# Optimization experiments

Hardware: AMD Instinct MI355X
Metric: run time of the kernel (lower is better)

Reference implementation:

```python
import jax, jax.numpy as jnp
import numpy as np

USER = 100000
ITEM = 200000
N = USER + ITEM
LATDIM = 64
N_LAYERS = 3
N_EDGES = 9600000


def setup_inputs() -> dict:
    key = jax.random.key(0)
    k1, k2, k3, k4, k5 = jax.random.split(key, 5)
    # xavier_uniform for [N, latdim]: bound = sqrt(6/(fan_in+fan_out))
    bu = float(np.sqrt(6.0 / (USER + LATDIM)))
    bi = float(np.sqrt(6.0 / (ITEM + LATDIM)))
    uEmbeds = jax.random.uniform(k1, (USER, LATDIM), jnp.float32, -bu, bu)
    iEmbeds = jax.random.uniform(k2, (ITEM, LATDIM), jnp.float32, -bi, bi)
    edge_row = jax.random.randint(k3, (N_EDGES,), 0, N, dtype=jnp.int32)
    edge_col = jax.random.randint(k4, (N_EDGES,), 0, N, dtype=jnp.int32)
    edge_val = jax.random.uniform(k5, (N_EDGES,), jnp.float32) * 0.01
    return {"uEmbeds": uEmbeds, "iEmbeds": iEmbeds,
            "edge_row": edge_row, "edge_col": edge_col, "edge_val": edge_val}


def _spmm(row, col, val, x):
    # sparse adj (COO) @ dense x: gather cols, scale, scatter-add to rows
    msgs = x[col] * val[:, None]                 # [E, D]
    return jax.ops.segment_sum(msgs, row, num_segments=N)  # [N, D]


def reference(uEmbeds, iEmbeds, edge_row, edge_col, edge_val):
    # forward_gcn: multi-layer propagation, sum of all layer embeddings
    embeds = jnp.concatenate([uEmbeds, iEmbeds], axis=0)  # [N, D]
    acc = embeds
    cur = embeds
    for _ in range(N_LAYERS):
        cur = _spmm(edge_row, edge_col, edge_val, cur)
        acc = acc + cur
    return acc[:USER], acc[USER:]
```

## Files before the change

kernel.cpp:

```cpp
#include <hip/hip_runtime.h>
#include <hip/hip_bf16.h>

#define USER_N   100000
#define ITEM_N   200000
#define N_NODES  300000
#define LATDIM   64
#define N_EDGES  9600000
#define N_LAYERS 3

#define B_SHIFT  6
#define B_ROWS   64
#define NB       ((N_NODES + B_ROWS - 1) / B_ROWS)
#define GPART    512
#define EPB      ((N_EDGES + GPART - 1) / GPART)
#define SEG      5
#define CAP      3072

__device__ __forceinline__ unsigned short f2bf(float f) {
    unsigned int u = __float_as_uint(f);
    u += 0x7FFFu + ((u >> 16) & 1u);
    return (unsigned short)(u >> 16);
}
__device__ __forceinline__ float bf2f(unsigned short h) {
    return __uint_as_float(((unsigned int)h) << 16);
}

__global__ void cvt_concat_kernel(const float* __restrict__ u,
                                  const float* __restrict__ it,
                                  ushort4* __restrict__ cur0,
                                  int n4u, int n4total) {
    int stride = gridDim.x * blockDim.x;
    for (int i = blockIdx.x * blockDim.x + threadIdx.x; i < n4total; i += stride) {
        float4 v = (i < n4u) ? ((const float4*)u)[i]
                             : ((const float4*)it)[i - n4u];
        ushort4 o;
        o.x = f2bf(v.x); o.y = f2bf(v.y); o.z = f2bf(v.z); o.w = f2bf(v.w);
        cur0[i] = o;
    }
}

__device__ __forceinline__ int slice_of(int blk) {
    return ((blk & 7) << 6) | (blk >> 3);
}

__global__ void p1_count_kernel(const int* __restrict__ row,
                                int* __restrict__ cnt) {
    __shared__ int h[NB];
    int s = slice_of(blockIdx.x), t = threadIdx.x;
    for (int i = t; i < NB; i += 256) h[i] = 0;
    __syncthreads();
    int e0 = s * EPB;
    int e1 = e0 + EPB; if (e1 > N_EDGES) e1 = N_EDGES;
    for (int e = e0 + t; e < e1; e += 256)
        atomicAdd(&h[row[e] >> B_SHIFT], 1);
    __syncthreads();
    for (int i = t; i < NB; i += 256)
        cnt[i * GPART + s] = h[i];
}

__global__ void p2_scan_kernel(int* __restrict__ cnt, int* __restrict__ btot) {
    __shared__ int lds[GPART];
    int b = blockIdx.x, t = threadIdx.x;
    int v = cnt[b * GPART + t];
    lds[t] = v;
    __syncthreads();
    for (int off = 1; off < GPART; off <<= 1) {
        int add = (t >= off) ? lds[t - off] : 0;
        __syncthreads();
        lds[t] += add;
        __syncthreads();
    }
    cnt[b * GPART + t] = lds[t] - v;
    if (t == GPART - 1) btot[b] = lds[t];
}

__global__ void p3_scan_kernel(const int* __restrict__ btot,
                               int* __restrict__ bstart,
                               int* __restrict__ rowPtr) {
    __shared__ int lds[1024];
    int t = threadIdx.x;
    int base = t * SEG;
    int loc[SEG];
    int s = 0;
    #pragma unroll
    for (int k = 0; k < SEG; ++k) {
        int i = base + k;
        int v = (i < NB) ? btot[i] : 0;
        loc[k] = v;
        s += v;
    }
    lds[t] = s;
    __syncthreads();
    for (int off = 1; off < 1024; off <<= 1) {
        int add = (t >= off) ? lds[t - off] : 0;
        __syncthreads();
        lds[t] += add;
        __syncthreads();
    }
    int ex = lds[t] - s;
    #pragma unroll
    for (int k = 0; k < SEG; ++k) {
        int i = base + k;
        if (i < NB) bstart[i] = ex;
        ex += loc[k];
    }
    if (t == 1023) {
        bstart[NB] = lds[1023];
        rowPtr[N_NODES] = N_EDGES;
    }
}

__global__ void p4_scatter_kernel(const int*   __restrict__ row,
                                  const int*   __restrict__ col,
                                  const float* __restrict__ val,
                                  const int*   __restrict__ bstart,
                                  const int*   __restrict__ cnt,
                                  int2*        __restrict__ temp) {
    __shared__ int cur[NB];
    int s = slice_of(blockIdx.x), t = threadIdx.x;
    for (int i = t; i < NB; i += 256)
        cur[i] = bstart[i] + cnt[i * GPART + s];
    __syncthreads();
    int e0 = s * EPB;
    int e1 = e0 + EPB; if (e1 > N_EDGES) e1 = N_EDGES;
    for (int e = e0 + t; e < e1; e += 256) {
        int r = row[e];
        int b = r >> B_SHIFT;
        int pos = atomicAdd(&cur[b], 1);
        temp[pos] = make_int2(((r & (B_ROWS - 1)) << 19) | col[e],
                              __float_as_int(val[e]));
    }
}

__global__ __launch_bounds__(256)
void bucket_sort_kernel(const int*  __restrict__ bstart,
                        const int2* __restrict__ temp,
                        int2*       __restrict__ colval,
                        int*        __restrict__ rowPtr) {
    __shared__ int hist[B_ROWS];
    __shared__ int curs[B_ROWS];
    __shared__ int2 stage[CAP];
    int b = blockIdx.x, t = threadIdx.x;
    int beg = bstart[b];
    int end = bstart[b + 1];
    int n = end - beg;

    if (t < B_ROWS) hist[t] = 0;
    __syncthreads();
    for (int i = beg + t; i < end; i += 256)
        atomicAdd(&hist[((unsigned)temp[i].x) >> 19], 1);
    __syncthreads();

    if (t < B_ROWS) {
        int v = hist[t];
        int inc = v;
        #pragma unroll
        for (int d = 1; d < B_ROWS; d <<= 1) {
            int o = __shfl_up(inc, d, 64);
            if (t >= d) inc += o;
        }
        int ex = inc - v;
        curs[t] = ex;
        int r = (b << B_SHIFT) + t;
        if (r < N_NODES) rowPtr[r] = beg + ex;
    }
    __syncthreads();

    for (int i = beg + t; i < end; i += 256) {
        int2 kv = temp[i];
        int rl = ((unsigned)kv.x) >> 19;
        int p  = atomicAdd(&curs[rl], 1);
        int2 out = make_int2(kv.x & 0x7FFFF, kv.y);
        if (p < CAP) stage[p] = out;
        else         colval[beg + p] = out;
    }
    __syncthreads();

    int lim = (n < CAP) ? n : CAP;
    for (int i = t; i < lim; i += 256)
        colval[beg + i] = stage[i];
}

__global__ void spmm_bf16_kernel(const int*  __restrict__ rp,
                                 const int2* __restrict__ cv,
                                 const ushort4* __restrict__ x4,
                                 ushort4*       __restrict__ y4) {
    int g = (blockIdx.x * blockDim.x + threadIdx.x) >> 4;
    if (g >= N_NODES) return;
    int q = threadIdx.x & 15;
    int beg = rp[g];
    int end = rp[g + 1];

    float s0 = 0.f, s1 = 0.f, s2 = 0.f, s3 = 0.f;
    int i = beg;
    for (; i + 4 <= end; i += 4) {
        int2 c0 = cv[i], c1 = cv[i + 1], c2 = cv[i + 2], c3 = cv[i + 3];
        ushort4 g0 = x4[(size_t)c0.x * 16 + q];
        ushort4 g1 = x4[(size_t)c1.x * 16 + q];
        ushort4 g2 = x4[(size_t)c2.x * 16 + q];
        ushort4 g3 = x4[(size_t)c3.x * 16 + q];
        float v0 = __int_as_float(c0.y), v1 = __int_as_float(c1.y);
        float v2 = __int_as_float(c2.y), v3 = __int_as_float(c3.y);
        s0 += bf2f(g0.x) * v0; s1 += bf2f(g0.y) * v0;
        s2 += bf2f(g0.z) * v0; s3 += bf2f(g0.w) * v0;
        s0 += bf2f(g1.x) * v1; s1 += bf2f(g1.y) * v1;
        s2 += bf2f(g1.z) * v1; s3 += bf2f(g1.w) * v1;
        s0 += bf2f(g2.x) * v2; s1 += bf2f(g2.y) * v2;
        s2 += bf2f(g2.z) * v2; s3 += bf2f(g2.w) * v2;
        s0 += bf2f(g3.x) * v3; s1 += bf2f(g3.y) * v3;
        s2 += bf2f(g3.z) * v3; s3 += bf2f(g3.w) * v3;
    }
    for (; i < end; ++i) {
        int2 cc = cv[i];
        ushort4 gg = x4[(size_t)cc.x * 16 + q];
        float v = __int_as_float(cc.y);
        s0 += bf2f(gg.x) * v; s1 += bf2f(gg.y) * v;
        s2 += bf2f(gg.z) * v; s3 += bf2f(gg.w) * v;
    }

    ushort4 o;
    o.x = f2bf(s0); o.y = f2bf(s1); o.z = f2bf(s2); o.w = f2bf(s3);
    y4[(size_t)g * 16 + q] = o;
}

__global__ void final_acc_kernel(const float* __restrict__ u,
                                 const float* __restrict__ it,
                                 const ushort4* __restrict__ c1,
                                 const ushort4* __restrict__ c2,
                                 const ushort4* __restrict__ c3,
                                 float4* __restrict__ acc,
                                 int n4u, int n4total) {
    int stride = gridDim.x * blockDim.x;
    for (int i = blockIdx.x * blockDim.x + threadIdx.x; i < n4total; i += stride) {
        float4 e = (i < n4u) ? ((const float4*)u)[i]
                             : ((const float4*)it)[i - n4u];
        ushort4 a = c1[i], b = c2[i], c = c3[i];
        e.x += bf2f(a.x) + bf2f(b.x) + bf2f(c.x);
        e.y += bf2f(a.y) + bf2f(b.y) + bf2f(c.y);
        e.z += bf2f(a.z) + bf2f(b.z) + bf2f(c.z);
        e.w += bf2f(a.w) + bf2f(b.w) + bf2f(c.w);
        acc[i] = e;
    }
}

__global__ void copy_concat_kernel(const float* __restrict__ u,
                                   const float* __restrict__ it,
                                   float* __restrict__ cur,
                                   float* __restrict__ acc,
                                   int n4u, int n4total) {
    int stride = gridDim.x * blockDim.x;
    for (int i = blockIdx.x * blockDim.x + threadIdx.x; i < n4total; i += stride) {
        float4 v = (i < n4u) ? ((const float4*)u)[i]
                             : ((const float4*)it)[i - n4u];
        ((float4*)cur)[i] = v;
        ((float4*)acc)[i] = v;
    }
}

__global__ void spmm_atomic_kernel(const int*   __restrict__ row,
                                   const int*   __restrict__ col,
                                   const float* __restrict__ val,
                                   const float* __restrict__ x,
                                   float*       __restrict__ y) {
    const int total = N_EDGES * 16;
    int stride = gridDim.x * blockDim.x;
    for (int t = blockIdx.x * blockDim.x + threadIdx.x; t < total; t += stride) {
        int e = t >> 4;
        int q = t & 15;
        int r = row[e];
        int c = col[e];
        float v = val[e];
        float4 g = ((const float4*)x)[c * 16 + q];
        float* yp = y + r * 64 + q * 4;
        atomicAdd(yp + 0, g.x * v);
        atomicAdd(yp + 1, g.y * v);
        atomicAdd(yp + 2, g.z * v);
        atomicAdd(yp + 3, g.w * v);
    }
}

__global__ void acc_add_kernel(float* __restrict__ acc,
                               const float* __restrict__ add,
                               int n4) {
    int stride = gridDim.x * blockDim.x;
    for (int i = blockIdx.x * blockDim.x + threadIdx.x; i < n4; i += stride) {
        float4 a = ((const float4*)acc)[i];
        float4 b = ((const float4*)add)[i];
        a.x += b.x; a.y += b.y; a.z += b.z; a.w += b.w;
        ((float4*)acc)[i] = a;
    }
}

extern "C" void kernel_launch(void* const* d_in, const int* in_sizes, int n_in,
                              void* d_out, int out_size, void* d_ws, size_t ws_size,
                              hipStream_t stream) {
    const float* uEmb = (const float*)d_in[0];
    const float* iEmb = (const float*)d_in[1];
    const int*   row  = (const int*)  d_in[2];
    const int*   col  = (const int*)  d_in[3];
    const float* val  = (const float*)d_in[4];

    float* acc = (float*)d_out;

    const int n4total = N_NODES * (LATDIM / 4);
    const int n4u     = USER_N  * (LATDIM / 4);
    const size_t embBytes  = (size_t)N_NODES * LATDIM * sizeof(float);
    const size_t embBytesH = (size_t)N_NODES * LATDIM * 2;

    const int BLK = 256;
    const int GRID_MEM = 2048;

    auto align256 = [](size_t x) { return (x + 255) & ~(size_t)255; };
    size_t off = 0;
    size_t o_cur0   = off; off += align256(embBytesH);
    size_t o_c1     = off; off += align256(embBytesH);
    size_t o_c2     = off; off += align256(embBytesH);
    size_t o_c3     = off; off += align256(embBytesH);
    size_t o_colval = off; off += align256((size_t)N_EDGES * 8);
    size_t o_rowptr = off; off += align256(((size_t)N_NODES + 1) * 4);
    size_t o_cnt    = off; off += align256((size_t)NB * GPART * 4);
    size_t o_btot   = off; off += align256((size_t)NB * 4);
    size_t o_bstart = off; off += align256(((size_t)NB + 1) * 4);
    size_t needed = off;

    char* wsb = (char*)d_ws;

    if (ws_size >= needed) {
        ushort4* cur0  = (ushort4*)(wsb + o_cur0);
        ushort4* c1    = (ushort4*)(wsb + o_c1);
        ushort4* c2    = (ushort4*)(wsb + o_c2);
        ushort4* c3    = (ushort4*)(wsb + o_c3);
        int2* colval = (int2*)(wsb + o_colval);
        int*  rowPtr = (int*) (wsb + o_rowptr);
        int*  cnt    = (int*) (wsb + o_cnt);
        int*  btot   = (int*) (wsb + o_btot);
        int*  bstart = (int*) (wsb + o_bstart);
        int2* temp   = (int2*)(wsb + o_c1);

        cvt_concat_kernel<<<GRID_MEM, BLK, 0, stream>>>(uEmb, iEmb, cur0,
                                                        n4u, n4total);

        p1_count_kernel  <<<GPART, 256, 0, stream>>>(row, cnt);
        p2_scan_kernel   <<<NB, GPART, 0, stream>>>(cnt, btot);
        p3_scan_kernel   <<<1, 1024, 0, stream>>>(btot, bstart, rowPtr);
        p4_scatter_kernel<<<GPART, 256, 0, stream>>>(row, col, val, bstart,
                                                     cnt, temp);
        bucket_sort_kernel<<<NB, 256, 0, stream>>>(bstart, temp, colval, rowPtr);

        const int GRID_SPMM = (N_NODES * 16 + BLK - 1) / BLK;
        spmm_bf16_kernel<<<GRID_SPMM, BLK, 0, stream>>>(rowPtr, colval, cur0, c1);
        spmm_bf16_kernel<<<GRID_SPMM, BLK, 0, stream>>>(rowPtr, colval, c1,   c2);
        spmm_bf16_kernel<<<GRID_SPMM, BLK, 0, stream>>>(rowPtr, colval, c2,   c3);

        final_acc_kernel<<<GRID_MEM, BLK, 0, stream>>>(uEmb, iEmb, c1, c2, c3,
                                                       (float4*)acc,
                                                       n4u, n4total);
    } else {
        float* cur = (float*)wsb;
        float* nxt = (float*)(wsb + embBytes);
        copy_concat_kernel<<<GRID_MEM, BLK, 0, stream>>>(uEmb, iEmb, cur, acc,
                                                         n4u, n4total);
        for (int l = 0; l < N_LAYERS; ++l) {
            hipMemsetAsync(nxt, 0, embBytes, stream);
            spmm_atomic_kernel<<<4096, BLK, 0, stream>>>(row, col, val, cur, nxt);
            acc_add_kernel<<<GRID_MEM, BLK, 0, stream>>>(acc, nxt, n4total);
            float* t = cur; cur = nxt; nxt = t;
        }
    }
}
```

Before: 926.1 us.

## Replace fine bucket CSR build with coarse two-pass radix partition and row atomics

Rebuilds the COO-to-CSR conversion. It now takes a per-row global histogram, a two-level scan over 4096-row coarse buckets, and a chunked LDS-staged scatter into coarse buckets. A second pass then places each edge in its row using per-row global atomic cursors. This replaces the 512-slice count matrix and the per-64-row bucket sort. It also unrolls the SpMM gather loop by 8 so more loads are in flight. Within a row, edge order now depends on atomic timing, so float summation order is nondeterministic. Global atomics on 300k row cursors may contend.

```diff
diff --git a/kernel.cpp b/kernel.cpp
--- a/kernel.cpp
+++ b/kernel.cpp
@@ -8,13 +8,13 @@
 #define N_EDGES  9600000
 #define N_LAYERS 3
 
-#define B_SHIFT  6
-#define B_ROWS   64
-#define NB       ((N_NODES + B_ROWS - 1) / B_ROWS)
-#define GPART    512
-#define EPB      ((N_EDGES + GPART - 1) / GPART)
-#define SEG      5
-#define CAP      3072
+#define CSHIFT   12
+#define CROWS    4096
+#define NCOARSE  ((N_NODES + CROWS - 1) / CROWS)
+#define NCPAD    80
+#define SUBS     64
+#define CHUNK    4096
+#define NCHUNKS  ((N_EDGES + CHUNK - 1) / CHUNK)
 
 __device__ __forceinline__ unsigned short f2bf(float f) {
     unsigned int u = __float_as_uint(f);
@@ -39,56 +39,66 @@
     }
 }
 
-__device__ __forceinline__ int slice_of(int blk) {
-    return ((blk & 7) << 6) | (blk >> 3);
-}
-
-__global__ void p1_count_kernel(const int* __restrict__ row,
-                                int* __restrict__ cnt) {
-    __shared__ int h[NB];
-    int s = slice_of(blockIdx.x), t = threadIdx.x;
-    for (int i = t; i < NB; i += 256) h[i] = 0;
+__global__ void hist_row_kernel(const int* __restrict__ row,
+                                int* __restrict__ counts) {
+    int stride = gridDim.x * blockDim.x;
+    for (int e = blockIdx.x * blockDim.x + threadIdx.x; e < N_EDGES; e += stride)
+        atomicAdd(&counts[row[e]], 1);
+}
+
+__global__ void coarse_sum_kernel(const int* __restrict__ counts,
+                                  int* __restrict__ csum) {
+    __shared__ int lds[1024];
+    int c = blockIdx.x, t = threadIdx.x;
+    int base = c * CROWS;
+    int s = 0;
+    #pragma unroll
+    for (int k = 0; k < 4; ++k) {
+        int i = base + t + k * 1024;
+        if (i < N_NODES) s += counts[i];
+    }
+    lds[t] = s;
     __syncthreads();
-    int e0 = s * EPB;
-    int e1 = e0 + EPB; if (e1 > N_EDGES) e1 = N_EDGES;
-    for (int e = e0 + t; e < e1; e += 256)
-        atomicAdd(&h[row[e] >> B_SHIFT], 1);
-    __syncthreads();
-    for (int i = t; i < NB; i += 256)
-        cnt[i * GPART + s] = h[i];
-}
-
-__global__ void p2_scan_kernel(int* __restrict__ cnt, int* __restrict__ btot) {
-    __shared__ int lds[GPART];
-    int b = blockIdx.x, t = threadIdx.x;
-    int v = cnt[b * GPART + t];
+    for (int off = 512; off > 0; off >>= 1) {
+        if (t < off) lds[t] += lds[t + off];
+        __syncthreads();
+    }
+    if (t == 0) csum[c] = lds[0];
+}
+
+__global__ void scan_coarse_kernel(const int* __restrict__ csum,
+                                   int* __restrict__ cbase,
+                                   int* __restrict__ cursorA,
+                                   int* __restrict__ rowPtr) {
+    __shared__ int lds[128];
+    int t = threadIdx.x;
+    int v = (t < NCOARSE) ? csum[t] : 0;
     lds[t] = v;
     __syncthreads();
-    for (int off = 1; off < GPART; off <<= 1) {
+    for (int off = 1; off < 128; off <<= 1) {
         int add = (t >= off) ? lds[t - off] : 0;
         __syncthreads();
         lds[t] += add;
         __syncthreads();
     }
-    cnt[b * GPART + t] = lds[t] - v;
-    if (t == GPART - 1) btot[b] = lds[t];
-}
-
-__global__ void p3_scan_kernel(const int* __restrict__ btot,
-                               int* __restrict__ bstart,
-                               int* __restrict__ rowPtr) {
+    if (t < NCOARSE) { int ex = lds[t] - v; cbase[t] = ex; cursorA[t] = ex; }
+    if (t == NCOARSE - 1) cbase[NCOARSE] = lds[t];
+    if (t == 0) rowPtr[N_NODES] = N_EDGES;
+}
+
+__global__ void scan_rows_kernel(const int* __restrict__ counts,
+                                 const int* __restrict__ cbase,
+                                 int* __restrict__ rowPtr,
+                                 int* __restrict__ rowCur) {
     __shared__ int lds[1024];
-    int t = threadIdx.x;
-    int base = t * SEG;
-    int loc[SEG];
-    int s = 0;
-    #pragma unroll
-    for (int k = 0; k < SEG; ++k) {
-        int i = base + k;
-        int v = (i < NB) ? btot[i] : 0;
-        loc[k] = v;
-        s += v;
-    }
+    int c = blockIdx.x, t = threadIdx.x;
+    int base = c * CROWS + t * 4;
+    int v0 = 0, v1 = 0, v2 = 0, v3 = 0;
+    if (base     < N_NODES) v0 = counts[base];
+    if (base + 1 < N_NODES) v1 = counts[base + 1];
+    if (base + 2 < N_NODES) v2 = counts[base + 2];
+    if (base + 3 < N_NODES) v3 = counts[base + 3];
+    int s = v0 + v1 + v2 + v3;
     lds[t] = s;
     __syncthreads();
     for (int off = 1; off < 1024; off <<= 1) {
@@ -97,88 +107,75 @@
         lds[t] += add;
         __syncthreads();
     }
-    int ex = lds[t] - s;
-    #pragma unroll
-    for (int k = 0; k < SEG; ++k) {
-        int i = base + k;
-        if (i < NB) bstart[i] = ex;
-        ex += loc[k];
-    }
-    if (t == 1023) {
-        bstart[NB] = lds[1023];
-        rowPtr[N_NODES] = N_EDGES;
-    }
-}
-
-__global__ void p4_scatter_kernel(const int*   __restrict__ row,
-                                  const int*   __restrict__ col,
-                                  const float* __restrict__ val,
-                                  const int*   __restrict__ bstart,
-                                  const int*   __restrict__ cnt,
-                                  int2*        __restrict__ temp) {
-    __shared__ int cur[NB];
-    int s = slice_of(blockIdx.x), t = threadIdx.x;
-    for (int i = t; i < NB; i += 256)
-        cur[i] = bstart[i] + cnt[i * GPART + s];
-    __syncthreads();
-    int e0 = s * EPB;
-    int e1 = e0 + EPB; if (e1 > N_EDGES) e1 = N_EDGES;
-    for (int e = e0 + t; e < e1; e += 256) {
-        int r = row[e];
-        int b = r >> B_SHIFT;
-        int pos = atomicAdd(&cur[b], 1);
-        temp[pos] = make_int2(((r & (B_ROWS - 1)) << 19) | col[e],
-                              __float_as_int(val[e]));
-    }
+    int ex = cbase[c] + lds[t] - s;
+    if (base     < N_NODES) { rowPtr[base]     = ex; rowCur[base]     = ex; } ex += v0;
+    if (base + 1 < N_NODES) { rowPtr[base + 1] = ex; rowCur[base + 1] = ex; } ex += v1;
+    if (base + 2 < N_NODES) { rowPtr[base + 2] = ex; rowCur[base + 2] = ex; } ex += v2;
+    if (base + 3 < N_NODES) { rowPtr[base + 3] = ex; rowCur[base + 3] = ex; }
 }
 
 __global__ __launch_bounds__(256)
-void bucket_sort_kernel(const int*  __restrict__ bstart,
-                        const int2* __restrict__ temp,
-                        int2*       __restrict__ colval,
-                        int*        __restrict__ rowPtr) {
-    __shared__ int hist[B_ROWS];
-    __shared__ int curs[B_ROWS];
-    __shared__ int2 stage[CAP];
-    int b = blockIdx.x, t = threadIdx.x;
-    int beg = bstart[b];
-    int end = bstart[b + 1];
+void passA_kernel(const int*   __restrict__ row,
+                  const int*   __restrict__ col,
+                  const float* __restrict__ val,
+                  int*         __restrict__ cursorA,
+                  int2*        __restrict__ tempA) {
+    __shared__ int2 stage[CHUNK];
+    __shared__ unsigned char cb[CHUNK];
+    __shared__ int h[NCOARSE];
+    __shared__ int cur[NCOARSE];
+    int t = threadIdx.x;
+    for (int cid = blockIdx.x; cid < NCHUNKS; cid += gridDim.x) {
+        if (t < NCOARSE) h[t] = 0;
+        __syncthreads();
+        int e0 = cid * CHUNK;
+        int e1 = e0 + CHUNK; if (e1 > N_EDGES) e1 = N_EDGES;
+        for (int e = e0 + t; e < e1; e += 256) {
+            int r = row[e];
+            int c = r >> CSHIFT;
+            stage[e - e0] = make_int2(((r & (CROWS - 1)) << 19) | col[e],
+                                      __float_as_int(val[e]));
+            cb[e - e0] = (unsigned char)c;
+            atomicAdd(&h[c], 1);
+        }
+        __syncthreads();
+        if (t < NCOARSE) {
+            int n = h[t];
+            cur[t] = n ? atomicAdd(&cursorA[t], n) : 0;
+        }
+        __syncthreads();
+        for (int e = e0 + t; e < e1; e += 256) {
+            int c = cb[e - e0];
+            int pos = atomicAdd(&cur[c], 1);
+            tempA[pos] = stage[e - e0];
+        }
+        __syncthreads();
+    }
+}
+
+__global__ __launch_bounds__(256)
+void passB_kernel(const int*  __restrict__ cbase,
+                  const int2* __restrict__ tempA,
+                  int*        __restrict__ rowCur,
+                  int2*       __restrict__ colval) {
+    int blk = blockIdx.x;
+    int x = blk & 7;
+    int j = blk >> 3;
+    int s = j & (SUBS - 1);
+    int c = (j >> 6) * 8 + x;
+    if (c >= NCOARSE) return;
+    int beg = cbase[c], end = cbase[c + 1];
     int n = end - beg;
-
-    if (t < B_ROWS) hist[t] = 0;
-    __syncthreads();
-    for (int i = beg + t; i < end; i += 256)
-        atomicAdd(&hist[((unsigned)temp[i].x) >> 19], 1);
-    __syncthreads();
-
-    if (t < B_ROWS) {
-        int v = hist[t];
-        int inc = v;
-        #pragma unroll
-        for (int d = 1; d < B_ROWS; d <<= 1) {
-            int o = __shfl_up(inc, d, 64);
-            if (t >= d) inc += o;
-        }
-        int ex = inc - v;
-        curs[t] = ex;
-        int r = (b << B_SHIFT) + t;
-        if (r < N_NODES) rowPtr[r] = beg + ex;
-    }
-    __syncthreads();
-
-    for (int i = beg + t; i < end; i += 256) {
-        int2 kv = temp[i];
-        int rl = ((unsigned)kv.x) >> 19;
-        int p  = atomicAdd(&curs[rl], 1);
-        int2 out = make_int2(kv.x & 0x7FFFF, kv.y);
-        if (p < CAP) stage[p] = out;
-        else         colval[beg + p] = out;
-    }
-    __syncthreads();
-
-    int lim = (n < CAP) ? n : CAP;
-    for (int i = t; i < lim; i += 256)
-        colval[beg + i] = stage[i];
+    int q = (n + SUBS - 1) / SUBS;
+    int i0 = beg + s * q;
+    int i1 = i0 + q; if (i1 > end) i1 = end;
+    int rbase = c << CSHIFT;
+    for (int i = i0 + threadIdx.x; i < i1; i += 256) {
+        int2 kv = tempA[i];
+        int r = rbase + (((unsigned)kv.x) >> 19);
+        int pos = atomicAdd(&rowCur[r], 1);
+        colval[pos] = make_int2(kv.x & 0x7FFFF, kv.y);
+    }
 }
 
 __global__ void spmm_bf16_kernel(const int*  __restrict__ rp,
@@ -193,22 +190,18 @@
 
     float s0 = 0.f, s1 = 0.f, s2 = 0.f, s3 = 0.f;
     int i = beg;
-    for (; i + 4 <= end; i += 4) {
-        int2 c0 = cv[i], c1 = cv[i + 1], c2 = cv[i + 2], c3 = cv[i + 3];
-        ushort4 g0 = x4[(size_t)c0.x * 16 + q];
-        ushort4 g1 = x4[(size_t)c1.x * 16 + q];
-        ushort4 g2 = x4[(size_t)c2.x * 16 + q];
-        ushort4 g3 = x4[(size_t)c3.x * 16 + q];
-        float v0 = __int_as_float(c0.y), v1 = __int_as_float(c1.y);
-        float v2 = __int_as_float(c2.y), v3 = __int_as_float(c3.y);
-        s0 += bf2f(g0.x) * v0; s1 += bf2f(g0.y) * v0;
-        s2 += bf2f(g0.z) * v0; s3 += bf2f(g0.w) * v0;
-        s0 += bf2f(g1.x) * v1; s1 += bf2f(g1.y) * v1;
-        s2 += bf2f(g1.z) * v1; s3 += bf2f(g1.w) * v1;
-        s0 += bf2f(g2.x) * v2; s1 += bf2f(g2.y) * v2;
-        s2 += bf2f(g2.z) * v2; s3 += bf2f(g2.w) * v2;
-        s0 += bf2f(g3.x) * v3; s1 += bf2f(g3.y) * v3;
-        s2 += bf2f(g3.z) * v3; s3 += bf2f(g3.w) * v3;
+    for (; i + 8 <= end; i += 8) {
+        int2 cc[8]; ushort4 gg[8];
+        #pragma unroll
+        for (int k = 0; k < 8; ++k) cc[k] = cv[i + k];
+        #pragma unroll
+        for (int k = 0; k < 8; ++k) gg[k] = x4[(size_t)cc[k].x * 16 + q];
+        #pragma unroll
+        for (int k = 0; k < 8; ++k) {
+            float v = __int_as_float(cc[k].y);
+            s0 += bf2f(gg[k].x) * v; s1 += bf2f(gg[k].y) * v;
+            s2 += bf2f(gg[k].z) * v; s3 += bf2f(gg[k].w) * v;
+        }
     }
     for (; i < end; ++i) {
         int2 cc = cv[i];
@@ -318,34 +311,41 @@
     size_t o_c3     = off; off += align256(embBytesH);
     size_t o_colval = off; off += align256((size_t)N_EDGES * 8);
     size_t o_rowptr = off; off += align256(((size_t)N_NODES + 1) * 4);
-    size_t o_cnt    = off; off += align256((size_t)NB * GPART * 4);
-    size_t o_btot   = off; off += align256((size_t)NB * 4);
-    size_t o_bstart = off; off += align256(((size_t)NB + 1) * 4);
+    size_t o_rowcur = off; off += align256((size_t)N_NODES * 4);
+    size_t o_counts = off; off += align256((size_t)N_NODES * 4);
+    size_t o_csum   = off; off += align256((size_t)NCOARSE * 4);
+    size_t o_cbase  = off; off += align256(((size_t)NCOARSE + 1) * 4);
+    size_t o_cursA  = off; off += align256((size_t)NCOARSE * 4);
     size_t needed = off;
 
     char* wsb = (char*)d_ws;
 
     if (ws_size >= needed) {
-        ushort4* cur0  = (ushort4*)(wsb + o_cur0);
-        ushort4* c1    = (ushort4*)(wsb + o_c1);
-        ushort4* c2    = (ushort4*)(wsb + o_c2);
-        ushort4* c3    = (ushort4*)(wsb + o_c3);
-        int2* colval = (int2*)(wsb + o_colval);
-        int*  rowPtr = (int*) (wsb + o_rowptr);
-        int*  cnt    = (int*) (wsb + o_cnt);
-        int*  btot   = (int*) (wsb + o_btot);
-        int*  bstart = (int*) (wsb + o_bstart);
-        int2* temp   = (int2*)(wsb + o_c1);
+        ushort4* cur0 = (ushort4*)(wsb + o_cur0);
+        ushort4* c1   = (ushort4*)(wsb + o_c1);
+        ushort4* c2   = (ushort4*)(wsb + o_c2);
+        ushort4* c3   = (ushort4*)(wsb + o_c3);
+        int2* colval  = (int2*)(wsb + o_colval);
+        int2* tempA   = (int2*)(wsb + o_c1);
+        int* rowPtr   = (int*)(wsb + o_rowptr);
+        int* rowCur   = (int*)(wsb + o_rowcur);
+        int* counts   = (int*)(wsb + o_counts);
+        int* csum     = (int*)(wsb + o_csum);
+        int* cbase    = (int*)(wsb + o_cbase);
+        int* cursorA  = (int*)(wsb + o_cursA);
 
         cvt_concat_kernel<<<GRID_MEM, BLK, 0, stream>>>(uEmb, iEmb, cur0,
                                                         n4u, n4total);
 
-        p1_count_kernel  <<<GPART, 256, 0, stream>>>(row, cnt);
-        p2_scan_kernel   <<<NB, GPART, 0, stream>>>(cnt, btot);
-        p3_scan_kernel   <<<1, 1024, 0, stream>>>(btot, bstart, rowPtr);
-        p4_scatter_kernel<<<GPART, 256, 0, stream>>>(row, col, val, bstart,
-                                                     cnt, temp);
-        bucket_sort_kernel<<<NB, 256, 0, stream>>>(bstart, temp, colval, rowPtr);
+        hipMemsetAsync(counts, 0, (size_t)N_NODES * 4, stream);
+        hist_row_kernel  <<<GRID_MEM, BLK, 0, stream>>>(row, counts);
+        coarse_sum_kernel<<<NCOARSE, 1024, 0, stream>>>(counts, csum);
+        scan_coarse_kernel<<<1, 128, 0, stream>>>(csum, cbase, cursorA, rowPtr);
+        scan_rows_kernel <<<NCOARSE, 1024, 0, stream>>>(counts, cbase,
+                                                        rowPtr, rowCur);
+        passA_kernel<<<1024, 256, 0, stream>>>(row, col, val, cursorA, tempA);
+        passB_kernel<<<8 * SUBS * (NCPAD / 8), 256, 0, stream>>>(cbase, tempA,
+                                                                 rowCur, colval);
 
         const int GRID_SPMM = (N_NODES * 16 + BLK - 1) / BLK;
         spmm_bf16_kernel<<<GRID_SPMM, BLK, 0, stream>>>(rowPtr, colval, cur0, c1);
```

New measurement: 1.413 ms. +52.6%, slower.
